# Kernel tuning notes

Measured on AMD Instinct MI355X. Metric: run time of the kernel, lower is better.

Reference implementation:

```python
import jax, jax.numpy as jnp
import numpy as np

FG_THRESH = 0.5

def _descriptors(fmap, scribbles):
    # fmap: [B, C, h, w]; scribbles: [B, I, H, W]
    B, C, h, w = fmap.shape
    I = scribbles.shape[1]
    # bilinear resize (align_corners=False == half-pixel, no antialias, like torch)
    sr = jax.image.resize(scribbles, (B, I, h, w), method='bilinear', antialias=False)
    mask = (sr > FG_THRESH).astype(fmap.dtype)                 # [B, I, h, w]
    cnt = mask.sum(axis=(-1, -2))                              # [B, I]
    ssum = jnp.einsum('bihw,bchw->bic', mask, fmap)            # masked sum over HW
    mean = ssum / jnp.maximum(cnt, 1.0)[..., None]             # [B, I, C]
    # fallback when a mask has no foreground pixels: feature at argmax of soft mask
    idx = jnp.argmax(sr.reshape(B, I, h * w), axis=-1)         # [B, I]
    fflat = fmap.reshape(B, C, h * w)
    fb = jnp.take_along_axis(fflat, idx[:, None, :], axis=2)   # [B, C, I]
    fb = fb.transpose(0, 2, 1)                                 # [B, I, C]
    return jnp.where((cnt > 0)[..., None], mean, fb)

def setup_inputs() -> dict:
    key = jax.random.key(0)
    k0, k1, k2, k3 = jax.random.split(key, 4)
    return {
        'feat0': jax.random.normal(k0, (8, 256, 128, 128), dtype=jnp.float32),
        'feat1': jax.random.normal(k1, (8, 256, 64, 64), dtype=jnp.float32),
        'feat2': jax.random.normal(k2, (8, 256, 32, 32), dtype=jnp.float32),
        'scribbles': jax.random.uniform(k3, (8, 16, 512, 512), dtype=jnp.float32),
    }

def reference(feat0, feat1, feat2, scribbles):
    # multi_scale=True, random_bg_queries=False: per-level masked mean pool,
    # then average descriptors across feature levels. Output: [B, I, C]
    d0 = _descriptors(feat0, scribbles)
    d1 = _descriptors(feat1, scribbles)
    d2 = _descriptors(feat2, scribbles)
    return (d0 + d1 + d2) / 3.0
```

## Files before the change

### kernel.cpp

```cpp
#include <hip/hip_runtime.h>
#include <stdint.h>

#define NB 8
#define NI 16
#define NC 256
#define SH 512
#define NCH 84

typedef __bf16 bf16x8 __attribute__((ext_vector_type(8)));
typedef float f32x4 __attribute__((ext_vector_type(4)));
typedef uint32_t u32x4 __attribute__((ext_vector_type(4)));

static const size_t OFF_SSP = 0;
static const size_t OFF_CNT = OFF_SSP + (size_t)NB * NCH * NI * NC * 4;
static const size_t OFF_KEY = OFF_CNT + (size_t)NB * NCH * NI * 4;
static const size_t WS_NEED = OFF_KEY + (size_t)NB * NCH * NI * 8;

__device__ __forceinline__ float4 ld4(const float* p) {
    return *reinterpret_cast<const float4*>(p);
}

__device__ __forceinline__ void mfma_step(const uint16_t* __restrict__ lmp, int ks, int cl,
                                          const float4 (&buf)[4][2],
                                          f32x4& a0, f32x4& a1, f32x4& a2, f32x4& a3) {
    const uint4 wA = *reinterpret_cast<const uint4*>(lmp + ks * 32);
    u32x4 au;
    au.x = ((wA.x >> cl) & 0x10001u) * 0x3F80u;
    au.y = ((wA.y >> cl) & 0x10001u) * 0x3F80u;
    au.z = ((wA.z >> cl) & 0x10001u) * 0x3F80u;
    au.w = ((wA.w >> cl) & 0x10001u) * 0x3F80u;
    const bf16x8 av = __builtin_bit_cast(bf16x8, au);
    #pragma unroll
    for (int nt = 0; nt < 4; ++nt) {
        bf16x8 bv;
        bv[0] = (__bf16)buf[nt][0].x; bv[1] = (__bf16)buf[nt][0].y;
        bv[2] = (__bf16)buf[nt][0].z; bv[3] = (__bf16)buf[nt][0].w;
        bv[4] = (__bf16)buf[nt][1].x; bv[5] = (__bf16)buf[nt][1].y;
        bv[6] = (__bf16)buf[nt][1].z; bv[7] = (__bf16)buf[nt][1].w;
        f32x4& ac = (nt == 0) ? a0 : (nt == 1) ? a1 : (nt == 2) ? a2 : a3;
        ac = __builtin_amdgcn_mfma_f32_16x16x32_bf16(av, bv, ac, 0, 0, 0);
    }
}

template<int W, int S, int P>
__device__ __forceinline__ void do_chunk(const float* __restrict__ f,
                                         const float* __restrict__ scr,
                                         float* __restrict__ ssp,
                                         int* __restrict__ cntp,
                                         unsigned long long* __restrict__ keyp,
                                         int b, int chunk, int slot, int tid,
                                         uint16_t* __restrict__ lmask,
                                         int* __restrict__ lcnt,
                                         unsigned long long* __restrict__ lkey) {
    const int wave = tid >> 6;
    const int lane = tid & 63;
    const int kg = lane >> 4;
    const int cl = lane & 15;
    const int c0 = wave * 64;
    const int kb = chunk * 256;
    const float* fp0 = f + ((size_t)b * NC + c0 + cl) * P + kb + kg * 8;
    float4 bA[4][2], bB[4][2];
    #pragma unroll
    for (int nt = 0; nt < 4; ++nt) {
        const float* fr = fp0 + (size_t)(nt * 16) * P;
        bA[nt][0] = ld4(fr);
        bA[nt][1] = ld4(fr + 4);
    }

    const int pix = chunk * 256 + tid;
    const int y = pix / W;
    const int x = pix - y * W;
    const int r0 = S * y + (S / 2 - 1);
    const int c0s = S * x + (S / 2 - 1);
    const float* sb = scr + (size_t)b * NI * (SH * SH) + (size_t)r0 * SH;
    unsigned int mword = 0;
    #pragma unroll
    for (int i = 0; i < NI; ++i) {
        const float* sp = sb + (size_t)i * (SH * SH);
        float s4;
        if constexpr (S == 4) {
            float4 q0 = ld4(sp + (c0s - 1));
            float4 q1 = ld4(sp + SH + (c0s - 1));
            s4 = (q0.y + q0.z) + (q1.y + q1.z);
        } else {
            s4 = (sp[c0s] + sp[c0s + 1]) + (sp[SH + c0s] + sp[SH + c0s + 1]);
        }
        bool bit = s4 > 2.0f;
        mword |= bit ? (1u << i) : 0u;
        unsigned long long bal = __ballot(bit);
        if (lane == 0) atomicAdd(&lcnt[i], (int)__popcll(bal));
        if (bal == 0ull) {
            unsigned int srb = __float_as_uint(0.25f * s4);
            unsigned int mx = srb;
            #pragma unroll
            for (int off = 1; off < 64; off <<= 1) {
                unsigned int o = __shfl_xor(mx, off, 64);
                mx = (o > mx) ? o : mx;
            }
            unsigned long long win = __ballot(srb == mx);
            if (lane == 0) {
                int wl = __ffsll((unsigned long long)win) - 1;
                unsigned int wpix = (unsigned int)(chunk * 256 + (tid & ~63) + wl);
                unsigned long long key = (((unsigned long long)mx) << 32)
                                       | (unsigned long long)(0xFFFFFFFFu - wpix);
                atomicMax(&lkey[i], key);
            }
        }
    }
    lmask[tid] = (uint16_t)mword;
    __syncthreads();
    if (tid < NI) {
        cntp[slot * NI + tid] = lcnt[tid];
        keyp[slot * NI + tid] = lkey[tid];
    }

    const uint16_t* lmp = lmask + kg * 8;
    f32x4 acc0 = {0.f, 0.f, 0.f, 0.f};
    f32x4 acc1 = {0.f, 0.f, 0.f, 0.f};
    f32x4 acc2 = {0.f, 0.f, 0.f, 0.f};
    f32x4 acc3 = {0.f, 0.f, 0.f, 0.f};
    #pragma unroll
    for (int ks = 0; ks < 8; ks += 2) {
        #pragma unroll
        for (int nt = 0; nt < 4; ++nt) {
            const float* fr = fp0 + (size_t)(nt * 16) * P + (ks + 1) * 32;
            bB[nt][0] = ld4(fr);
            bB[nt][1] = ld4(fr + 4);
        }
        mfma_step(lmp, ks, cl, bA, acc0, acc1, acc2, acc3);
        if (ks + 2 < 8) {
            #pragma unroll
            for (int nt = 0; nt < 4; ++nt) {
                const float* fr = fp0 + (size_t)(nt * 16) * P + (ks + 2) * 32;
                bA[nt][0] = ld4(fr);
                bA[nt][1] = ld4(fr + 4);
            }
        }
        mfma_step(lmp, ks + 1, cl, bB, acc0, acc1, acc2, acc3);
    }
    float* sb2 = ssp + (size_t)slot * (NI * NC);
    #pragma unroll
    for (int nt = 0; nt < 4; ++nt) {
        const f32x4 ac = (nt == 0) ? acc0 : (nt == 1) ? acc1 : (nt == 2) ? acc2 : acc3;
        const int c = c0 + nt * 16 + cl;
        #pragma unroll
        for (int r = 0; r < 4; ++r)
            sb2[(kg * 4 + r) * NC + c] = ac[r];
    }
}

__global__ __launch_bounds__(256, 2) void fused_kernel(const float* __restrict__ f0,
                                                       const float* __restrict__ f1,
                                                       const float* __restrict__ f2,
                                                       const float* __restrict__ scr,
                                                       float* __restrict__ ssp,
                                                       int* __restrict__ cntp,
                                                       unsigned long long* __restrict__ keyp) {
    __shared__ __align__(16) uint16_t lmask[256];
    __shared__ int lcnt[NI];
    __shared__ unsigned long long lkey[NI];
    const int tid = threadIdx.x;
    const int b = blockIdx.y;
    const int bx = blockIdx.x;
    if (tid < NI) { lcnt[tid] = 0; lkey[tid] = 0ull; }
    __syncthreads();
    const int slot = b * NCH + bx;
    if (bx < 64) {
        do_chunk<128, 4, 16384>(f0, scr, ssp, cntp, keyp, b, bx, slot, tid,
                                lmask, lcnt, lkey);
    } else if (bx < 80) {
        do_chunk<64, 8, 4096>(f1, scr, ssp, cntp, keyp, b, bx - 64, slot, tid,
                              lmask, lcnt, lkey);
    } else {
        do_chunk<32, 16, 1024>(f2, scr, ssp, cntp, keyp, b, bx - 80, slot, tid,
                               lmask, lcnt, lkey);
    }
}

__global__ __launch_bounds__(256) void final_kernel(const float* __restrict__ f0,
                                                    const float* __restrict__ f1,
                                                    const float* __restrict__ f2,
                                                    const int* __restrict__ cntp,
                                                    const unsigned long long* __restrict__ keyp,
                                                    const float* __restrict__ ssp,
                                                    float* __restrict__ out) {
    __shared__ int scnt[3];
    __shared__ unsigned long long skey[3];
    __shared__ float red[4][64];
    const int bi = blockIdx.x;
    const int cq = blockIdx.y;
    const int b = bi >> 4;
    const int i = bi & 15;
    const int tid = threadIdx.x;
    const int cl = tid & 63;
    const int jg = tid >> 6;
    const int CH[3] = {64, 16, 4};
    const int O[3] = {0, 64, 80};
    if (tid < 3) { scnt[tid] = 0; skey[tid] = 0ull; }
    __syncthreads();
    if (tid < NCH) {
        int l = (tid < 64) ? 0 : (tid < 80) ? 1 : 2;
        const int slot = b * NCH + tid;
        atomicAdd(&scnt[l], cntp[slot * NI + i]);
        atomicMax(&skey[l], keyp[slot * NI + i]);
    }
    __syncthreads();
    const float* fl[3] = {f0, f1, f2};
    const int Ps[3] = {16384, 4096, 1024};
    float r = 0.f;
    #pragma unroll
    for (int l = 0; l < 3; ++l) {
        const int cn = scnt[l];
        if (cn > 0) {
            float s = 0.f;
            for (int j = jg; j < CH[l]; j += 4)
                s += ssp[((size_t)(b * NCH + O[l] + j) * NI + i) * NC + cq * 64 + cl];
            red[jg][cl] = s;
            __syncthreads();
            if (jg == 0)
                r += ((red[0][cl] + red[1][cl]) + (red[2][cl] + red[3][cl])) / (float)cn;
            __syncthreads();
        } else if (jg == 0) {
            unsigned int p = 0xFFFFFFFFu - (unsigned int)(skey[l] & 0xFFFFFFFFull);
            r += fl[l][((size_t)b * NC + cq * 64 + cl) * Ps[l] + p];
        }
    }
    if (jg == 0) out[(size_t)bi * NC + cq * 64 + cl] = r * (1.f / 3.f);
}

extern "C" void kernel_launch(void* const* d_in, const int* in_sizes, int n_in,
                              void* d_out, int out_size, void* d_ws, size_t ws_size,
                              hipStream_t stream) {
    const float* f0  = (const float*)d_in[0];
    const float* f1  = (const float*)d_in[1];
    const float* f2  = (const float*)d_in[2];
    const float* scr = (const float*)d_in[3];
    float* out = (float*)d_out;
    char* ws = (char*)d_ws;
    if (ws_size < WS_NEED) return;

    float* ssp = (float*)(ws + OFF_SSP);
    int* cntp = (int*)(ws + OFF_CNT);
    unsigned long long* keyp = (unsigned long long*)(ws + OFF_KEY);

    fused_kernel<<<dim3(NCH, NB), 256, 0, stream>>>(f0, f1, f2, scr, ssp, cntp, keyp);
    final_kernel<<<dim3(NB * NI, 4), 256, 0, stream>>>(f0, f1, f2, cntp, keyp, ssp, out);
}
```

Measured before the change: 69.61 us.

## Double block size to split scribble channels and feature columns across more waves

The fused kernel now runs 512 threads per block instead of 256. Each half of the block samples 8 of the 16 scribble channels, and the two 8-bit masks are merged in shared memory into the 16-bit mask. Each of the 8 waves now handles 32 feature channels instead of 64, which halves the per-thread loads and MFMAs and the register footprint. The intent is more memory-level parallelism and latency hiding in this load-bound kernel, at the cost of an extra barrier and the shared-memory merge step.

```diff
diff --git a/kernel.cpp b/kernel.cpp
--- a/kernel.cpp
+++ b/kernel.cpp
@@ -21,8 +21,8 @@
 }
 
 __device__ __forceinline__ void mfma_step(const uint16_t* __restrict__ lmp, int ks, int cl,
-                                          const float4 (&buf)[4][2],
-                                          f32x4& a0, f32x4& a1, f32x4& a2, f32x4& a3) {
+                                          const float4 (&buf)[2][2],
+                                          f32x4& a0, f32x4& a1) {
     const uint4 wA = *reinterpret_cast<const uint4*>(lmp + ks * 32);
     u32x4 au;
     au.x = ((wA.x >> cl) & 0x10001u) * 0x3F80u;
@@ -31,13 +31,13 @@
     au.w = ((wA.w >> cl) & 0x10001u) * 0x3F80u;
     const bf16x8 av = __builtin_bit_cast(bf16x8, au);
     #pragma unroll
-    for (int nt = 0; nt < 4; ++nt) {
+    for (int nt = 0; nt < 2; ++nt) {
         bf16x8 bv;
         bv[0] = (__bf16)buf[nt][0].x; bv[1] = (__bf16)buf[nt][0].y;
         bv[2] = (__bf16)buf[nt][0].z; bv[3] = (__bf16)buf[nt][0].w;
         bv[4] = (__bf16)buf[nt][1].x; bv[5] = (__bf16)buf[nt][1].y;
         bv[6] = (__bf16)buf[nt][1].z; bv[7] = (__bf16)buf[nt][1].w;
-        f32x4& ac = (nt == 0) ? a0 : (nt == 1) ? a1 : (nt == 2) ? a2 : a3;
+        f32x4& ac = (nt == 0) ? a0 : a1;
         ac = __builtin_amdgcn_mfma_f32_16x16x32_bf16(av, bv, ac, 0, 0, 0);
     }
 }
@@ -49,33 +49,36 @@
                                          int* __restrict__ cntp,
                                          unsigned long long* __restrict__ keyp,
                                          int b, int chunk, int slot, int tid,
-                                         uint16_t* __restrict__ lmask,
+                                         uint8_t* __restrict__ lmask8,
+                                         uint16_t* __restrict__ lmask16,
                                          int* __restrict__ lcnt,
                                          unsigned long long* __restrict__ lkey) {
     const int wave = tid >> 6;
     const int lane = tid & 63;
     const int kg = lane >> 4;
     const int cl = lane & 15;
-    const int c0 = wave * 64;
+    const int c0 = wave * 32;
     const int kb = chunk * 256;
     const float* fp0 = f + ((size_t)b * NC + c0 + cl) * P + kb + kg * 8;
-    float4 bA[4][2], bB[4][2];
-    #pragma unroll
-    for (int nt = 0; nt < 4; ++nt) {
+    float4 bA[2][2], bB[2][2];
+    #pragma unroll
+    for (int nt = 0; nt < 2; ++nt) {
         const float* fr = fp0 + (size_t)(nt * 16) * P;
         bA[nt][0] = ld4(fr);
         bA[nt][1] = ld4(fr + 4);
     }
 
-    const int pix = chunk * 256 + tid;
+    const int gi = tid >> 8;
+    const int p = tid & 255;
+    const int pix = chunk * 256 + p;
     const int y = pix / W;
     const int x = pix - y * W;
     const int r0 = S * y + (S / 2 - 1);
     const int c0s = S * x + (S / 2 - 1);
-    const float* sb = scr + (size_t)b * NI * (SH * SH) + (size_t)r0 * SH;
+    const float* sb = scr + ((size_t)b * NI + gi * 8) * (SH * SH) + (size_t)r0 * SH;
     unsigned int mword = 0;
     #pragma unroll
-    for (int i = 0; i < NI; ++i) {
+    for (int i = 0; i < 8; ++i) {
         const float* sp = sb + (size_t)i * (SH * SH);
         float s4;
         if constexpr (S == 4) {
@@ -88,7 +91,7 @@
         bool bit = s4 > 2.0f;
         mword |= bit ? (1u << i) : 0u;
         unsigned long long bal = __ballot(bit);
-        if (lane == 0) atomicAdd(&lcnt[i], (int)__popcll(bal));
+        if (lane == 0) atomicAdd(&lcnt[gi * 8 + i], (int)__popcll(bal));
         if (bal == 0ull) {
             unsigned int srb = __float_as_uint(0.25f * s4);
             unsigned int mx = srb;
@@ -100,48 +103,49 @@
             unsigned long long win = __ballot(srb == mx);
             if (lane == 0) {
                 int wl = __ffsll((unsigned long long)win) - 1;
-                unsigned int wpix = (unsigned int)(chunk * 256 + (tid & ~63) + wl);
+                unsigned int wpix = (unsigned int)(chunk * 256 + (p & ~63) + wl);
                 unsigned long long key = (((unsigned long long)mx) << 32)
                                        | (unsigned long long)(0xFFFFFFFFu - wpix);
-                atomicMax(&lkey[i], key);
+                atomicMax(&lkey[gi * 8 + i], key);
             }
         }
     }
-    lmask[tid] = (uint16_t)mword;
-    __syncthreads();
+    lmask8[gi * 256 + p] = (uint8_t)mword;
+    __syncthreads();
+    if (tid < 256)
+        lmask16[tid] = (uint16_t)(lmask8[tid] | ((unsigned)lmask8[256 + tid] << 8));
     if (tid < NI) {
         cntp[slot * NI + tid] = lcnt[tid];
         keyp[slot * NI + tid] = lkey[tid];
     }
-
-    const uint16_t* lmp = lmask + kg * 8;
+    __syncthreads();
+
+    const uint16_t* lmp = lmask16 + kg * 8;
     f32x4 acc0 = {0.f, 0.f, 0.f, 0.f};
     f32x4 acc1 = {0.f, 0.f, 0.f, 0.f};
-    f32x4 acc2 = {0.f, 0.f, 0.f, 0.f};
-    f32x4 acc3 = {0.f, 0.f, 0.f, 0.f};
     #pragma unroll
     for (int ks = 0; ks < 8; ks += 2) {
         #pragma unroll
-        for (int nt = 0; nt < 4; ++nt) {
+        for (int nt = 0; nt < 2; ++nt) {
             const float* fr = fp0 + (size_t)(nt * 16) * P + (ks + 1) * 32;
             bB[nt][0] = ld4(fr);
             bB[nt][1] = ld4(fr + 4);
         }
-        mfma_step(lmp, ks, cl, bA, acc0, acc1, acc2, acc3);
+        mfma_step(lmp, ks, cl, bA, acc0, acc1);
         if (ks + 2 < 8) {
             #pragma unroll
-            for (int nt = 0; nt < 4; ++nt) {
+            for (int nt = 0; nt < 2; ++nt) {
                 const float* fr = fp0 + (size_t)(nt * 16) * P + (ks + 2) * 32;
                 bA[nt][0] = ld4(fr);
                 bA[nt][1] = ld4(fr + 4);
             }
         }
-        mfma_step(lmp, ks + 1, cl, bB, acc0, acc1, acc2, acc3);
+        mfma_step(lmp, ks + 1, cl, bB, acc0, acc1);
     }
     float* sb2 = ssp + (size_t)slot * (NI * NC);
     #pragma unroll
-    for (int nt = 0; nt < 4; ++nt) {
-        const f32x4 ac = (nt == 0) ? acc0 : (nt == 1) ? acc1 : (nt == 2) ? acc2 : acc3;
+    for (int nt = 0; nt < 2; ++nt) {
+        const f32x4 ac = (nt == 0) ? acc0 : acc1;
         const int c = c0 + nt * 16 + cl;
         #pragma unroll
         for (int r = 0; r < 4; ++r)
@@ -149,14 +153,15 @@
     }
 }
 
-__global__ __launch_bounds__(256, 2) void fused_kernel(const float* __restrict__ f0,
-                                                       const float* __restrict__ f1,
-                                                       const float* __restrict__ f2,
-                                                       const float* __restrict__ scr,
-                                                       float* __restrict__ ssp,
-                                                       int* __restrict__ cntp,
-                                                       unsigned long long* __restrict__ keyp) {
-    __shared__ __align__(16) uint16_t lmask[256];
+__global__ __launch_bounds__(512) void fused_kernel(const float* __restrict__ f0,
+                                                    const float* __restrict__ f1,
+                                                    const float* __restrict__ f2,
+                                                    const float* __restrict__ scr,
+                                                    float* __restrict__ ssp,
+                                                    int* __restrict__ cntp,
+                                                    unsigned long long* __restrict__ keyp) {
+    __shared__ uint8_t lmask8[512];
+    __shared__ __align__(16) uint16_t lmask16[256];
     __shared__ int lcnt[NI];
     __shared__ unsigned long long lkey[NI];
     const int tid = threadIdx.x;
@@ -167,13 +172,13 @@
     const int slot = b * NCH + bx;
     if (bx < 64) {
         do_chunk<128, 4, 16384>(f0, scr, ssp, cntp, keyp, b, bx, slot, tid,
-                                lmask, lcnt, lkey);
+                                lmask8, lmask16, lcnt, lkey);
     } else if (bx < 80) {
         do_chunk<64, 8, 4096>(f1, scr, ssp, cntp, keyp, b, bx - 64, slot, tid,
-                              lmask, lcnt, lkey);
+                              lmask8, lmask16, lcnt, lkey);
     } else {
         do_chunk<32, 16, 1024>(f2, scr, ssp, cntp, keyp, b, bx - 80, slot, tid,
-                               lmask, lcnt, lkey);
+                               lmask8, lmask16, lcnt, lkey);
     }
 }
 
@@ -243,6 +248,6 @@
     int* cntp = (int*)(ws + OFF_CNT);
     unsigned long long* keyp = (unsigned long long*)(ws + OFF_KEY);
 
-    fused_kernel<<<dim3(NCH, NB), 256, 0, stream>>>(f0, f1, f2, scr, ssp, cntp, keyp);
+    fused_kernel<<<dim3(NCH, NB), 512, 0, stream>>>(f0, f1, f2, scr, ssp, cntp, keyp);
     final_kernel<<<dim3(NB * NI, 4), 256, 0, stream>>>(f0, f1, f2, cntp, keyp, ssp, out);
 }
```

Measured after the change: 63.72 us. 8.5% less time.
